# Kernel tuning notes

Measured on AMD Instinct MI355X. Metric: run time of the kernel, lower is better.

Reference implementation:

```python
import jax, jax.numpy as jnp
import numpy as np

NEG_SLOPE = 0.01  # torch F.leaky_relu default


def setup_inputs() -> dict:
    key = jax.random.key(0)
    k1, k2, k3, k4 = jax.random.split(key, 4)
    B, N, F_in, F_out = 16, 2048, 128, 128
    stdv = 1.0 / np.sqrt(F_out)
    h = jax.random.normal(k1, (B, N, F_in), dtype=jnp.float32)
    adj = jax.random.uniform(k2, (B, N, N), dtype=jnp.float32)
    W = jax.random.uniform(k3, (F_in, F_out), minval=-stdv, maxval=stdv, dtype=jnp.float32)
    a = jax.random.uniform(k4, (2 * F_out, 1), minval=-stdv, maxval=stdv, dtype=jnp.float32)
    return {"h": h, "adj": adj, "W": W, "a": a}


def reference(h, adj, W, a):
    # Wh: [B, N, F_out]
    Wh = jnp.matmul(h, W)
    F_out = W.shape[1]
    a1 = a[:F_out, 0]  # [F_out]
    a2 = a[F_out:, 0]  # [F_out]
    # concat-score factorizes: e[b,i,j] = leaky(Wh[b,i]@a1 + Wh[b,j]@a2)
    f1 = jnp.einsum('bnf,f->bn', Wh, a1)  # [B, N]
    f2 = jnp.einsum('bnf,f->bn', Wh, a2)  # [B, N]
    e = jax.nn.leaky_relu(f1[:, :, None] + f2[:, None, :], negative_slope=NEG_SLOPE)  # [B,N,N]
    # NOTE: original softmax is over dim=1 (row index i), faithfully preserved
    attention = jax.nn.softmax(e, axis=1)
    h_prime = jnp.einsum('bij,bjf->bif', attention, Wh)  # bmm
    return h_prime
```

## Files before the change

kernel.cpp:

```cpp
#include <hip/hip_runtime.h>

#define BB 16
#define NN 2048
#define FF 128
#define NEG 0.01f

__global__ __launch_bounds__(256) void k_wh(const float* __restrict__ h,
                                            const float* __restrict__ Wg,
                                            const float* __restrict__ a,
                                            float* __restrict__ Wh,
                                            float* __restrict__ f1,
                                            float* __restrict__ f2) {
    __shared__ float Ws[64 * 128];
    __shared__ float hsT[64 * 36];

    const int tid  = threadIdx.x;
    const int fg   = tid & 31;
    const int slot = tid >> 5;
    const int f4   = fg * 4;
    const int rowBase = blockIdx.x * 32;

    float acc[4][4];
#pragma unroll
    for (int r = 0; r < 4; ++r)
#pragma unroll
        for (int c = 0; c < 4; ++c) acc[r][c] = 0.f;

    const float4* Wg4 = (const float4*)Wg;
    const float4* hg4 = (const float4*)h;

    for (int kh = 0; kh < 128; kh += 64) {
        __syncthreads();
        for (int idx = tid; idx < 64 * 32; idx += 256) {
            int kk = idx >> 5, ff = idx & 31;
            ((float4*)Ws)[kk * 32 + ff] = Wg4[(size_t)(kh + kk) * 32 + ff];
        }
#pragma unroll
        for (int pass = 0; pass < 2; ++pass) {
            int idx = pass * 256 + tid;
            int kq = idx & 15, row = idx >> 4;
            float4 h4 = hg4[(size_t)(rowBase + row) * 32 + (kh >> 2) + kq];
            hsT[(kq * 4 + 0) * 36 + row] = h4.x;
            hsT[(kq * 4 + 1) * 36 + row] = h4.y;
            hsT[(kq * 4 + 2) * 36 + row] = h4.z;
            hsT[(kq * 4 + 3) * 36 + row] = h4.w;
        }
        __syncthreads();
#pragma unroll 8
        for (int kk = 0; kk < 64; ++kk) {
            float4 wv = *(const float4*)&Ws[kk * 128 + f4];
            float4 hv = *(const float4*)&hsT[kk * 36 + slot * 4];
            acc[0][0] += hv.x * wv.x; acc[0][1] += hv.x * wv.y; acc[0][2] += hv.x * wv.z; acc[0][3] += hv.x * wv.w;
            acc[1][0] += hv.y * wv.x; acc[1][1] += hv.y * wv.y; acc[1][2] += hv.y * wv.z; acc[1][3] += hv.y * wv.w;
            acc[2][0] += hv.z * wv.x; acc[2][1] += hv.z * wv.y; acc[2][2] += hv.z * wv.z; acc[2][3] += hv.z * wv.w;
            acc[3][0] += hv.w * wv.x; acc[3][1] += hv.w * wv.y; acc[3][2] += hv.w * wv.z; acc[3][3] += hv.w * wv.w;
        }
    }

    const float4* ag4 = (const float4*)a;
    float4 a1v = ag4[fg];
    float4 a2v = ag4[32 + fg];

#pragma unroll
    for (int r = 0; r < 4; ++r) {
        int row = rowBase + slot * 4 + r;
        float4 o; o.x = acc[r][0]; o.y = acc[r][1]; o.z = acc[r][2]; o.w = acc[r][3];
        *(float4*)&Wh[(size_t)row * 128 + f4] = o;
        float p1 = acc[r][0] * a1v.x + acc[r][1] * a1v.y + acc[r][2] * a1v.z + acc[r][3] * a1v.w;
        float p2 = acc[r][0] * a2v.x + acc[r][1] * a2v.y + acc[r][2] * a2v.z + acc[r][3] * a2v.w;
#pragma unroll
        for (int m = 16; m >= 1; m >>= 1) {
            p1 += __shfl_xor(p1, m);
            p2 += __shfl_xor(p2, m);
        }
        if (fg == 0) { f1[row] = p1; f2[row] = p2; }
    }
}

__global__ __launch_bounds__(1024) void k_sort(const float* __restrict__ f1,
                                               const float* __restrict__ f2,
                                               float* __restrict__ Uarr,
                                               float* __restrict__ Warr,
                                               int* __restrict__ PERM,
                                               int* __restrict__ KIDX) {
    __shared__ float sKey[NN];
    __shared__ int   sIdx[NN];
    __shared__ float sSF1[NN];
    __shared__ float bufA[NN];
    __shared__ float bufB[NN];
    __shared__ float sPA[NN + 1];
    __shared__ float sSA[NN + 1];

    const int tid = threadIdx.x;
    const int b   = blockIdx.x;
    const float* f1b = f1 + b * NN;
    const float* f2b = f2 + b * NN;

    for (int i = tid; i < NN; i += 1024) sKey[i] = f1b[i];
    __syncthreads();
    for (int k = 2; k <= NN; k <<= 1) {
        for (int j = k >> 1; j > 0; j >>= 1) {
            int mask = j - 1;
            int i = ((tid & ~mask) << 1) | (tid & mask);
            int ixj = i | j;
            bool up = ((i & k) == 0);
            float av = sKey[i], bv = sKey[ixj];
            if ((av > bv) == up) { sKey[i] = bv; sKey[ixj] = av; }
            __syncthreads();
        }
    }
    for (int i = tid; i < NN; i += 1024) sSF1[i] = sKey[i];
    __syncthreads();

    for (int i = tid; i < NN; i += 1024) bufA[i] = expf(NEG * sSF1[i]);
    {
        float* s = bufA; float* d = bufB;
        for (int dd = 1; dd < NN; dd <<= 1) {
            __syncthreads();
            for (int i = tid; i < NN; i += 1024) {
                float v = s[i];
                if (i >= dd) v += s[i - dd];
                d[i] = v;
            }
            float* t = s; s = d; d = t;
        }
        __syncthreads();
        for (int i = tid; i < NN; i += 1024) sPA[i + 1] = s[i];
        if (tid == 0) sPA[0] = 0.f;
    }
    __syncthreads();

    for (int i = tid; i < NN; i += 1024) bufA[i] = expf(sSF1[NN - 1 - i]);
    {
        float* s = bufA; float* d = bufB;
        for (int dd = 1; dd < NN; dd <<= 1) {
            __syncthreads();
            for (int i = tid; i < NN; i += 1024) {
                float v = s[i];
                if (i >= dd) v += s[i - dd];
                d[i] = v;
            }
            float* t = s; s = d; d = t;
        }
        __syncthreads();
        for (int i = tid; i < NN; i += 1024) sSA[NN - 1 - i] = s[i];
        if (tid == 0) sSA[NN] = 0.f;
    }
    __syncthreads();

    for (int i = tid; i < NN; i += 1024) { sKey[i] = f2b[i]; sIdx[i] = i; }
    __syncthreads();
    for (int k = 2; k <= NN; k <<= 1) {
        for (int j = k >> 1; j > 0; j >>= 1) {
            int mask = j - 1;
            int i = ((tid & ~mask) << 1) | (tid & mask);
            int ixj = i | j;
            bool up = ((i & k) == 0);
            float av = sKey[i], bv = sKey[ixj];
            if ((av > bv) == up) {
                sKey[i] = bv; sKey[ixj] = av;
                int t2 = sIdx[i]; sIdx[i] = sIdx[ixj]; sIdx[ixj] = t2;
            }
            __syncthreads();
        }
    }

    for (int t = tid; t < NN; t += 1024) {
        float f2v = sKey[t];
        float tau = -f2v;
        int lo = 0, hi = NN;
        while (lo < hi) { int m = (lo + hi) >> 1; if (sSF1[m] <= tau) lo = m + 1; else hi = m; }
        float eS = expf(NEG * f2v);
        float eF = expf(f2v);
        float D = eS * sPA[lo] + eF * sSA[lo];
        float inv = 1.0f / D;
        Uarr[b * NN + t] = eF * inv;
        Warr[b * NN + t] = eS * inv;
        PERM[b * NN + t] = sIdx[t];
    }

    for (int i = tid; i < NN; i += 1024) {
        float tau = -f1b[i];
        int lo = 0, hi = NN;
        while (lo < hi) { int m = (lo + hi) >> 1; if (sKey[m] <= tau) lo = m + 1; else hi = m; }
        KIDX[b * NN + i] = lo;
    }
}

__global__ __launch_bounds__(128) void k_chunk(const float* __restrict__ Wh,
                                               const float* __restrict__ Uarr,
                                               const float* __restrict__ Warr,
                                               const int* __restrict__ PERM,
                                               float* __restrict__ CU,
                                               float* __restrict__ CW) {
    int blk = blockIdx.x;
    int b = blk >> 4, c = blk & 15;
    int f = threadIdx.x;
    int base = b * NN + c * 128;
    const float* Whb = Wh + (size_t)b * NN * FF;
    float aU = 0.f, aW = 0.f;
#pragma unroll 4
    for (int t = 0; t < 128; ++t) {
        int j = PERM[base + t];
        float uv = Uarr[base + t], wv = Warr[base + t];
        float whv = Whb[(size_t)j * FF + f];
        aU += uv * whv; aW += wv * whv;
    }
    CU[(size_t)blk * 128 + f] = aU;
    CW[(size_t)blk * 128 + f] = aW;
}

__global__ __launch_bounds__(128) void k_offsets(float* __restrict__ CU,
                                                 float* __restrict__ CW) {
    int b = blockIdx.x, f = threadIdx.x;
    float aU = 0.f, aW = 0.f;
#pragma unroll
    for (int c = 0; c < 16; ++c) {
        size_t idx = (size_t)(b * 16 + c) * 128 + f;
        float tU = CU[idx], tW = CW[idx];
        CU[idx] = aU; CW[idx] = aW;
        aU += tU; aW += tW;
    }
}

__global__ __launch_bounds__(128) void k_prefix(const float* __restrict__ Wh,
                                                const float* __restrict__ Uarr,
                                                const float* __restrict__ Warr,
                                                const int* __restrict__ PERM,
                                                const float* __restrict__ CU,
                                                const float* __restrict__ CW,
                                                float* __restrict__ PU,
                                                float* __restrict__ PW) {
    int blk = blockIdx.x;
    int b = blk >> 4, c = blk & 15;
    int f = threadIdx.x;
    int base = b * NN + c * 128;
    const float* Whb = Wh + (size_t)b * NN * FF;
    float aU = CU[(size_t)blk * 128 + f];
    float aW = CW[(size_t)blk * 128 + f];
    size_t rowB = (size_t)b * (NN + 1);
#pragma unroll 4
    for (int t = 0; t < 128; ++t) {
        int g = c * 128 + t;
        PU[(rowB + g) * FF + f] = aU;
        PW[(rowB + g) * FF + f] = aW;
        int j = PERM[base + t];
        float whv = Whb[(size_t)j * FF + f];
        aU += Uarr[base + t] * whv;
        aW += Warr[base + t] * whv;
    }
    if (c == 15) {
        PU[(rowB + NN) * FF + f] = aU;
        PW[(rowB + NN) * FF + f] = aW;
    }
}

__global__ __launch_bounds__(256) void k_out(const float* __restrict__ PU,
                                             const float* __restrict__ PW,
                                             const float* __restrict__ f1,
                                             const int* __restrict__ KIDX,
                                             float* __restrict__ out) {
    int rowId = blockIdx.x * 2 + (threadIdx.x >> 7);
    int f = threadIdx.x & 127;
    int b = rowId >> 11;
    int k = KIDX[rowId];
    float f1v = f1[rowId];
    float alpha = expf(NEG * f1v);
    float beta  = expf(f1v);
    size_t rowB = (size_t)b * (NN + 1);
    float totU = PU[(rowB + NN) * FF + f];
    float pu   = PU[(rowB + k) * FF + f];
    float pw   = PW[(rowB + k) * FF + f];
    out[(size_t)rowId * FF + f] = alpha * pw + beta * (totU - pu);
}

extern "C" void kernel_launch(void* const* d_in, const int* in_sizes, int n_in,
                              void* d_out, int out_size, void* d_ws, size_t ws_size,
                              hipStream_t stream) {
    const float* h  = (const float*)d_in[0];
    const float* W  = (const float*)d_in[2];
    const float* a  = (const float*)d_in[3];
    float* out = (float*)d_out;

    float* ws = (float*)d_ws;
    float* Wh   = ws;  ws += (size_t)BB * NN * FF;
    float* f1   = ws;  ws += BB * NN;
    float* f2   = ws;  ws += BB * NN;
    float* Uarr = ws;  ws += BB * NN;
    float* Warr = ws;  ws += BB * NN;
    float* CU   = ws;  ws += BB * 16 * FF;
    float* CW   = ws;  ws += BB * 16 * FF;
    float* PU   = ws;  ws += (size_t)BB * (NN + 1) * FF;
    float* PW   = ws;  ws += (size_t)BB * (NN + 1) * FF;
    int* PERM = (int*)ws;  ws += BB * NN;
    int* KIDX = (int*)ws;

    k_wh     <<<(BB * NN) / 32, 256, 0, stream>>>(h, W, a, Wh, f1, f2);
    k_sort   <<<BB, 1024, 0, stream>>>(f1, f2, Uarr, Warr, PERM, KIDX);
    k_chunk  <<<BB * 16, 128, 0, stream>>>(Wh, Uarr, Warr, PERM, CU, CW);
    k_offsets<<<BB, 128, 0, stream>>>(CU, CW);
    k_prefix <<<BB * 16, 128, 0, stream>>>(Wh, Uarr, Warr, PERM, CU, CW, PU, PW);
    k_out    <<<(BB * NN) / 2, 256, 0, stream>>>(PU, PW, f1, KIDX, out);
}
```

Before: 408.1 us.

## Split sort into parallel per-key blocks, wave-level scans, and finer prefix chunks

The single per-batch sort kernel becomes two blocks per batch, one sorting f1 and one sorting f2 with indices, so both bitonic sorts run concurrently. Bitonic stages with stride below 128 use a wave barrier instead of a block barrier. The log-step shared-memory scans are replaced by wavefront shuffle scans. A separate small kernel computes the U/W normalisers, and the chunked prefix kernels now use 32 chunks instead of 16 for more parallelism. The cost is an extra launch and global round-trips for the sorted arrays and scans.

```diff
diff --git a/kernel.cpp b/kernel.cpp
--- a/kernel.cpp
+++ b/kernel.cpp
@@ -4,6 +4,8 @@
 #define NN 2048
 #define FF 128
 #define NEG 0.01f
+#define CH 32
+#define CL (NN / CH)
 
 __global__ __launch_bounds__(256) void k_wh(const float* __restrict__ h,
                                             const float* __restrict__ Wg,
@@ -77,113 +79,134 @@
     }
 }
 
-__global__ __launch_bounds__(1024) void k_sort(const float* __restrict__ f1,
-                                               const float* __restrict__ f2,
-                                               float* __restrict__ Uarr,
-                                               float* __restrict__ Warr,
-                                               int* __restrict__ PERM,
-                                               int* __restrict__ KIDX) {
+__device__ __forceinline__ float wave_incl_scan(float s, int lane) {
+#pragma unroll
+    for (int m = 1; m <= 32; m <<= 1) {
+        float o = __shfl_up(s, m);
+        if (lane >= m) s += o;
+    }
+    return s;
+}
+
+#define WAVE_SYNC() do { __builtin_amdgcn_wave_barrier(); asm volatile("" ::: "memory"); } while (0)
+
+__global__ __launch_bounds__(1024) void k_sort2(const float* __restrict__ f1,
+                                                const float* __restrict__ f2,
+                                                float* __restrict__ SF1g,
+                                                float* __restrict__ PAg,
+                                                float* __restrict__ SAg,
+                                                float* __restrict__ SKg,
+                                                int* __restrict__ PERM,
+                                                int* __restrict__ KIDX) {
     __shared__ float sKey[NN];
     __shared__ int   sIdx[NN];
-    __shared__ float sSF1[NN];
-    __shared__ float bufA[NN];
-    __shared__ float bufB[NN];
-    __shared__ float sPA[NN + 1];
-    __shared__ float sSA[NN + 1];
-
-    const int tid = threadIdx.x;
-    const int b   = blockIdx.x;
+    __shared__ float wtot[16];
+
+    const int tid  = threadIdx.x;
+    const int lane = tid & 63;
+    const int w    = tid >> 6;
+    const int b    = blockIdx.x & 15;
+    const int task = blockIdx.x >> 4;
+
     const float* f1b = f1 + b * NN;
     const float* f2b = f2 + b * NN;
 
-    for (int i = tid; i < NN; i += 1024) sKey[i] = f1b[i];
-    __syncthreads();
+    if (task == 0) {
+        for (int i = tid; i < NN; i += 1024) sKey[i] = f1b[i];
+    } else {
+        for (int i = tid; i < NN; i += 1024) { sKey[i] = f2b[i]; sIdx[i] = i; }
+    }
+
+    int prevj = 1024;
     for (int k = 2; k <= NN; k <<= 1) {
         for (int j = k >> 1; j > 0; j >>= 1) {
+            if (j >= 128 || prevj >= 128) __syncthreads();
+            else WAVE_SYNC();
             int mask = j - 1;
-            int i = ((tid & ~mask) << 1) | (tid & mask);
-            int ixj = i | j;
-            bool up = ((i & k) == 0);
-            float av = sKey[i], bv = sKey[ixj];
-            if ((av > bv) == up) { sKey[i] = bv; sKey[ixj] = av; }
-            __syncthreads();
-        }
-    }
-    for (int i = tid; i < NN; i += 1024) sSF1[i] = sKey[i];
-    __syncthreads();
-
-    for (int i = tid; i < NN; i += 1024) bufA[i] = expf(NEG * sSF1[i]);
-    {
-        float* s = bufA; float* d = bufB;
-        for (int dd = 1; dd < NN; dd <<= 1) {
-            __syncthreads();
-            for (int i = tid; i < NN; i += 1024) {
-                float v = s[i];
-                if (i >= dd) v += s[i - dd];
-                d[i] = v;
-            }
-            float* t = s; s = d; d = t;
-        }
-        __syncthreads();
-        for (int i = tid; i < NN; i += 1024) sPA[i + 1] = s[i];
-        if (tid == 0) sPA[0] = 0.f;
-    }
-    __syncthreads();
-
-    for (int i = tid; i < NN; i += 1024) bufA[i] = expf(sSF1[NN - 1 - i]);
-    {
-        float* s = bufA; float* d = bufB;
-        for (int dd = 1; dd < NN; dd <<= 1) {
-            __syncthreads();
-            for (int i = tid; i < NN; i += 1024) {
-                float v = s[i];
-                if (i >= dd) v += s[i - dd];
-                d[i] = v;
-            }
-            float* t = s; s = d; d = t;
-        }
-        __syncthreads();
-        for (int i = tid; i < NN; i += 1024) sSA[NN - 1 - i] = s[i];
-        if (tid == 0) sSA[NN] = 0.f;
-    }
-    __syncthreads();
-
-    for (int i = tid; i < NN; i += 1024) { sKey[i] = f2b[i]; sIdx[i] = i; }
-    __syncthreads();
-    for (int k = 2; k <= NN; k <<= 1) {
-        for (int j = k >> 1; j > 0; j >>= 1) {
-            int mask = j - 1;
-            int i = ((tid & ~mask) << 1) | (tid & mask);
+            int i   = ((tid & ~mask) << 1) | (tid & mask);
             int ixj = i | j;
             bool up = ((i & k) == 0);
             float av = sKey[i], bv = sKey[ixj];
             if ((av > bv) == up) {
                 sKey[i] = bv; sKey[ixj] = av;
-                int t2 = sIdx[i]; sIdx[i] = sIdx[ixj]; sIdx[ixj] = t2;
+                if (task == 1) { int t2 = sIdx[i]; sIdx[i] = sIdx[ixj]; sIdx[ixj] = t2; }
             }
+            prevj = j;
+        }
+    }
+    __syncthreads();
+
+    if (task == 0) {
+        for (int i = tid; i < NN; i += 1024) SF1g[b * NN + i] = sKey[i];
+        const size_t pbase = (size_t)b * (NN + 1);
+        {
+            float a0 = expf(NEG * sKey[2 * tid]);
+            float a1 = expf(NEG * sKey[2 * tid + 1]);
+            float s = a0 + a1;
+            float v = wave_incl_scan(s, lane);
+            if (lane == 63) wtot[w] = v;
             __syncthreads();
-        }
-    }
-
-    for (int t = tid; t < NN; t += 1024) {
-        float f2v = sKey[t];
+            float off = 0.f;
+#pragma unroll
+            for (int ww = 0; ww < 16; ++ww) off += (ww < w) ? wtot[ww] : 0.f;
+            float excl = off + v - s;
+            PAg[pbase + 2 * tid]     = excl;
+            PAg[pbase + 2 * tid + 1] = excl + a0;
+            if (tid == 1023) PAg[pbase + NN] = off + v;
+        }
+        __syncthreads();
+        {
+            float y0 = expf(sKey[NN - 1 - 2 * tid]);
+            float y1 = expf(sKey[NN - 2 - 2 * tid]);
+            float s = y0 + y1;
+            float v = wave_incl_scan(s, lane);
+            if (lane == 63) wtot[w] = v;
+            __syncthreads();
+            float off = 0.f;
+#pragma unroll
+            for (int ww = 0; ww < 16; ++ww) off += (ww < w) ? wtot[ww] : 0.f;
+            SAg[pbase + NN - 1 - 2 * tid] = off + (v - s) + y0;
+            SAg[pbase + NN - 2 - 2 * tid] = off + v;
+            if (tid == 0) SAg[pbase + NN] = 0.f;
+        }
+    } else {
+        for (int i = tid; i < NN; i += 1024) {
+            SKg[b * NN + i]  = sKey[i];
+            PERM[b * NN + i] = sIdx[i];
+        }
+        for (int i = tid; i < NN; i += 1024) {
+            float tau = -f1b[i];
+            int lo = 0, hi = NN;
+            while (lo < hi) { int m = (lo + hi) >> 1; if (sKey[m] <= tau) lo = m + 1; else hi = m; }
+            KIDX[b * NN + i] = lo;
+        }
+    }
+}
+
+__global__ __launch_bounds__(256) void k_uw(const float* __restrict__ SF1g,
+                                            const float* __restrict__ PAg,
+                                            const float* __restrict__ SAg,
+                                            const float* __restrict__ SKg,
+                                            float* __restrict__ Uarr,
+                                            float* __restrict__ Warr) {
+    __shared__ float sS[NN];
+    __shared__ float sP[NN + 1];
+    __shared__ float sA[NN + 1];
+    const int b = blockIdx.x, tid = threadIdx.x;
+    const size_t pbase = (size_t)b * (NN + 1);
+    for (int i = tid; i < NN; i += 256) sS[i] = SF1g[b * NN + i];
+    for (int i = tid; i < NN + 1; i += 256) { sP[i] = PAg[pbase + i]; sA[i] = SAg[pbase + i]; }
+    __syncthreads();
+    for (int t = tid; t < NN; t += 256) {
+        float f2v = SKg[b * NN + t];
         float tau = -f2v;
         int lo = 0, hi = NN;
-        while (lo < hi) { int m = (lo + hi) >> 1; if (sSF1[m] <= tau) lo = m + 1; else hi = m; }
+        while (lo < hi) { int m = (lo + hi) >> 1; if (sS[m] <= tau) lo = m + 1; else hi = m; }
         float eS = expf(NEG * f2v);
         float eF = expf(f2v);
-        float D = eS * sPA[lo] + eF * sSA[lo];
-        float inv = 1.0f / D;
+        float inv = 1.0f / (eS * sP[lo] + eF * sA[lo]);
         Uarr[b * NN + t] = eF * inv;
         Warr[b * NN + t] = eS * inv;
-        PERM[b * NN + t] = sIdx[t];
-    }
-
-    for (int i = tid; i < NN; i += 1024) {
-        float tau = -f1b[i];
-        int lo = 0, hi = NN;
-        while (lo < hi) { int m = (lo + hi) >> 1; if (sKey[m] <= tau) lo = m + 1; else hi = m; }
-        KIDX[b * NN + i] = lo;
     }
 }
 
@@ -194,13 +217,13 @@
                                                float* __restrict__ CU,
                                                float* __restrict__ CW) {
     int blk = blockIdx.x;
-    int b = blk >> 4, c = blk & 15;
+    int b = blk / CH, c = blk % CH;
     int f = threadIdx.x;
-    int base = b * NN + c * 128;
+    int base = b * NN + c * CL;
     const float* Whb = Wh + (size_t)b * NN * FF;
     float aU = 0.f, aW = 0.f;
 #pragma unroll 4
-    for (int t = 0; t < 128; ++t) {
+    for (int t = 0; t < CL; ++t) {
         int j = PERM[base + t];
         float uv = Uarr[base + t], wv = Warr[base + t];
         float whv = Whb[(size_t)j * FF + f];
@@ -215,8 +238,8 @@
     int b = blockIdx.x, f = threadIdx.x;
     float aU = 0.f, aW = 0.f;
 #pragma unroll
-    for (int c = 0; c < 16; ++c) {
-        size_t idx = (size_t)(b * 16 + c) * 128 + f;
+    for (int c = 0; c < CH; ++c) {
+        size_t idx = (size_t)(b * CH + c) * 128 + f;
         float tU = CU[idx], tW = CW[idx];
         CU[idx] = aU; CW[idx] = aW;
         aU += tU; aW += tW;
@@ -232,16 +255,16 @@
                                                 float* __restrict__ PU,
                                                 float* __restrict__ PW) {
     int blk = blockIdx.x;
-    int b = blk >> 4, c = blk & 15;
+    int b = blk / CH, c = blk % CH;
     int f = threadIdx.x;
-    int base = b * NN + c * 128;
+    int base = b * NN + c * CL;
     const float* Whb = Wh + (size_t)b * NN * FF;
     float aU = CU[(size_t)blk * 128 + f];
     float aW = CW[(size_t)blk * 128 + f];
     size_t rowB = (size_t)b * (NN + 1);
 #pragma unroll 4
-    for (int t = 0; t < 128; ++t) {
-        int g = c * 128 + t;
+    for (int t = 0; t < CL; ++t) {
+        int g = c * CL + t;
         PU[(rowB + g) * FF + f] = aU;
         PW[(rowB + g) * FF + f] = aW;
         int j = PERM[base + t];
@@ -249,7 +272,7 @@
         aU += Uarr[base + t] * whv;
         aW += Warr[base + t] * whv;
     }
-    if (c == 15) {
+    if (c == CH - 1) {
         PU[(rowB + NN) * FF + f] = aU;
         PW[(rowB + NN) * FF + f] = aW;
     }
@@ -286,19 +309,24 @@
     float* Wh   = ws;  ws += (size_t)BB * NN * FF;
     float* f1   = ws;  ws += BB * NN;
     float* f2   = ws;  ws += BB * NN;
+    float* SF1  = ws;  ws += BB * NN;
+    float* PA   = ws;  ws += BB * (NN + 1);
+    float* SA   = ws;  ws += BB * (NN + 1);
+    float* SK   = ws;  ws += BB * NN;
     float* Uarr = ws;  ws += BB * NN;
     float* Warr = ws;  ws += BB * NN;
-    float* CU   = ws;  ws += BB * 16 * FF;
-    float* CW   = ws;  ws += BB * 16 * FF;
+    float* CU   = ws;  ws += BB * CH * FF;
+    float* CW   = ws;  ws += BB * CH * FF;
     float* PU   = ws;  ws += (size_t)BB * (NN + 1) * FF;
     float* PW   = ws;  ws += (size_t)BB * (NN + 1) * FF;
     int* PERM = (int*)ws;  ws += BB * NN;
     int* KIDX = (int*)ws;
 
     k_wh     <<<(BB * NN) / 32, 256, 0, stream>>>(h, W, a, Wh, f1, f2);
-    k_sort   <<<BB, 1024, 0, stream>>>(f1, f2, Uarr, Warr, PERM, KIDX);
-    k_chunk  <<<BB * 16, 128, 0, stream>>>(Wh, Uarr, Warr, PERM, CU, CW);
+    k_sort2  <<<2 * BB, 1024, 0, stream>>>(f1, f2, SF1, PA, SA, SK, PERM, KIDX);
+    k_uw     <<<BB, 256, 0, stream>>>(SF1, PA, SA, SK, Uarr, Warr);
+    k_chunk  <<<BB * CH, 128, 0, stream>>>(Wh, Uarr, Warr, PERM, CU, CW);
     k_offsets<<<BB, 128, 0, stream>>>(CU, CW);
-    k_prefix <<<BB * 16, 128, 0, stream>>>(Wh, Uarr, Warr, PERM, CU, CW, PU, PW);
+    k_prefix <<<BB * CH, 128, 0, stream>>>(Wh, Uarr, Warr, PERM, CU, CW, PU, PW);
     k_out    <<<(BB * NN) / 2, 256, 0, stream>>>(PU, PW, f1, KIDX, out);
 }
```

Result: faster. 390.9 us (-4.2%).
